# Kernel tuning notes

Measured on AMD Instinct MI355X. Metric: run time of the kernel, lower is better.

Reference implementation:

```python
import jax, jax.numpy as jnp
import numpy as np

ROPE_BASE = 10000.0


def _rope_tables(T, d, dtype):
    # inv_freq over even indices, emb = concat(freqs, freqs) -> [T, d]
    inv_freq = 1.0 / (ROPE_BASE ** (jnp.arange(0, d, 2, dtype=jnp.float32) / d))
    t = jnp.arange(T, dtype=jnp.float32)
    freqs = jnp.einsum('i,j->ij', t, inv_freq)          # [T, d/2]
    emb = jnp.concatenate([freqs, freqs], axis=-1)      # [T, d]
    return jnp.cos(emb).astype(dtype), jnp.sin(emb).astype(dtype)


def _rotate_half(x):
    d = x.shape[-1] // 2
    return jnp.concatenate([-x[..., d:], x[..., :d]], axis=-1)


def _apply_rope(x, cos, sin):
    # x: [B, T, H, Dh]; cos/sin: [T, Dh] broadcast over batch and heads
    c = cos[None, :, None, :]
    s = sin[None, :, None, :]
    return x * c + _rotate_half(x) * s


def setup_inputs() -> dict:
    key = jax.random.key(0)
    k1, k2, k3 = jax.random.split(key, 3)
    B, T, C = 2, 2048, 1024
    x = jax.random.normal(k1, (B, T, C), dtype=jnp.float32)
    # weights stored as [in, out] (transposed nn.Linear), scaled like torch init
    W_qkv = jax.random.normal(k2, (C, 3 * C), dtype=jnp.float32) * (C ** -0.5)
    W_proj = jax.random.normal(k3, (C, C), dtype=jnp.float32) * (C ** -0.5)
    return {'x': x, 'W_qkv': W_qkv, 'W_proj': W_proj}


def reference(x, W_qkv, W_proj):
    B, T, C = x.shape
    H = 16
    Dh = C // H
    qkv = x @ W_qkv                                   # [B, T, 3C]
    q, k, v = jnp.split(qkv, 3, axis=-1)
    q = q.reshape(B, T, H, Dh)
    k = k.reshape(B, T, H, Dh)
    v = v.reshape(B, T, H, Dh)
    cos, sin = _rope_tables(T, Dh, x.dtype)
    q = _apply_rope(q, cos, sin)
    k = _apply_rope(k, cos, sin)
    scale = 1.0 / jnp.sqrt(jnp.asarray(Dh, dtype=x.dtype))
    # causal SDPA: scores [B, H, T, T]
    scores = jnp.einsum('bqhd,bkhd->bhqk', q, k) * scale
    causal = jnp.tril(jnp.ones((T, T), dtype=bool))
    scores = jnp.where(causal[None, None], scores, jnp.asarray(-jnp.inf, dtype=scores.dtype))
    attn = jax.nn.softmax(scores, axis=-1)
    y = jnp.einsum('bhqk,bkhd->bqhd', attn, v).reshape(B, T, C)
    return y @ W_proj
```

## Files before the change

kernel.cpp:

```cpp
#include <hip/hip_runtime.h>
#include <cstdint>
#include <cstddef>

typedef __bf16 bf16;
typedef __bf16 bf16x2 __attribute__((ext_vector_type(2)));
typedef __bf16 bf16x4 __attribute__((ext_vector_type(4)));
typedef __bf16 bf16x8 __attribute__((ext_vector_type(8)));
typedef float  f32x4  __attribute__((ext_vector_type(4)));
typedef float  f32x16 __attribute__((ext_vector_type(16)));
typedef int    i32x4  __attribute__((ext_vector_type(4)));

__device__ __forceinline__ float fexp2(float x) {
  float r;
  asm("v_exp_f32 %0, %1" : "=v"(r) : "v"(x));
  return r;
}
__device__ __forceinline__ float m3(float a, float b, float c) {
  return fmaxf(fmaxf(a, b), c);
}

#define G2L(src, dst)                                                          \
  __builtin_amdgcn_global_load_lds(                                            \
      (const __attribute__((address_space(1))) unsigned int*)(src),            \
      (__attribute__((address_space(3))) unsigned int*)(dst), 16, 0, 0)

__global__ void k_conv_tables(const float* __restrict__ in, bf16* __restrict__ out,
                              float* __restrict__ cosT, float* __restrict__ sinT) {
  int bx = blockIdx.x;
  if (bx < 2048) {
    int i = (bx * 256 + threadIdx.x) * 8;
    float4 a = *(const float4*)(in + i);
    float4 b = *(const float4*)(in + i + 4);
    bf16x8 o;
    o[0] = (bf16)a.x; o[1] = (bf16)a.y; o[2] = (bf16)a.z; o[3] = (bf16)a.w;
    o[4] = (bf16)b.x; o[5] = (bf16)b.y; o[6] = (bf16)b.z; o[7] = (bf16)b.w;
    *(bf16x8*)(out + i) = o;
  } else {
    int i = (bx - 2048) * 256 + threadIdx.x;
    int t = i >> 5, j = i & 31;
    float inv = powf(10000.0f, -(float)j * (1.0f / 32.0f));
    float f = (float)t * inv;
    cosT[i] = cosf(f);
    sinT[i] = sinf(f);
  }
}

__global__ void k_transpose_w(const float* __restrict__ wqkv, bf16* __restrict__ wqkvt,
                              const float* __restrict__ wproj, bf16* __restrict__ wprojt) {
  __shared__ float tile[32][33];
  int bx = blockIdx.x;
  const float* in;
  bf16* out;
  int C;
  if (bx < 96) { in = wqkv; out = wqkvt; C = 3072; }
  else         { in = wproj; out = wprojt; C = 1024; bx -= 96; }
  const int R = 1024;
  int c0 = bx * 32, r0 = blockIdx.y * 32;
  int tx = threadIdx.x & 31, ty = threadIdx.x >> 5;
#pragma unroll
  for (int i = 0; i < 32; i += 8)
    tile[ty + i][tx] = in[(size_t)(r0 + ty + i) * C + c0 + tx];
  __syncthreads();
#pragma unroll
  for (int i = 0; i < 32; i += 8)
    out[(size_t)(c0 + ty + i) * R + r0 + tx] = (bf16)tile[tx][ty + i];
}

__global__ __launch_bounds__(256) void k_rope_v(const bf16* __restrict__ qkv,
                                                const float* __restrict__ cosT,
                                                const float* __restrict__ sinT,
                                                bf16* __restrict__ qr,
                                                bf16* __restrict__ kr,
                                                bf16* __restrict__ vt) {
  __shared__ bf16 tile[64][66];
  int bh = blockIdx.y;
  int t0 = blockIdx.x * 64;
  int b = bh >> 4, h = bh & 15;
  int tt = threadIdx.x >> 2, g = threadIdx.x & 3;
  int c4 = g * 16;
  const bf16* row = qkv + (size_t)(b * 2048 + t0 + tt) * 3072 + h * 64;
  bf16x8 v0 = *(const bf16x8*)(row + 2048 + c4);
  bf16x8 v1 = *(const bf16x8*)(row + 2048 + c4 + 8);
#pragma unroll
  for (int j = 0; j < 8; j++) { tile[tt][c4 + j] = v0[j]; tile[tt][c4 + 8 + j] = v1[j]; }
  int tglob = t0 + tt;
  size_t ob = ((size_t)bh * 2048 + tglob) * 64;
  const float QS = 0.125f * 1.44269504f;
  bf16x8 qlo = *(const bf16x8*)(row + g * 8);
  bf16x8 qhi = *(const bf16x8*)(row + 32 + g * 8);
  bf16x8 klo = *(const bf16x8*)(row + 1024 + g * 8);
  bf16x8 khi = *(const bf16x8*)(row + 1024 + 32 + g * 8);
  bf16x8 qo0, qo1, ko0, ko1;
#pragma unroll
  for (int j = 0; j < 8; j++) {
    float c = cosT[tglob * 32 + g * 8 + j], s = sinT[tglob * 32 + g * 8 + j];
    float ql = (float)qlo[j], qh = (float)qhi[j];
    float kl = (float)klo[j], kh = (float)khi[j];
    qo0[j] = (bf16)((ql * c - qh * s) * QS);
    qo1[j] = (bf16)((qh * c + ql * s) * QS);
    ko0[j] = (bf16)(kl * c - kh * s);
    ko1[j] = (bf16)(kh * c + kl * s);
  }
  *(bf16x8*)&qr[ob + g * 8]      = qo0;
  *(bf16x8*)&qr[ob + 32 + g * 8] = qo1;
  *(bf16x8*)&kr[ob + g * 8]      = ko0;
  *(bf16x8*)&kr[ob + 32 + g * 8] = ko1;
  __syncthreads();
  int d = threadIdx.x >> 2, tc0 = (threadIdx.x & 3) * 16;
  bf16x8 o0, o1;
#pragma unroll
  for (int j = 0; j < 8; j++) { o0[j] = tile[tc0 + j][d]; o1[j] = tile[tc0 + 8 + j][d]; }
  bf16* dst = vt + ((size_t)bh * 64 + d) * 2048 + t0 + tc0;
  *(bf16x8*)dst = o0;
  *(bf16x8*)(dst + 8) = o1;
}

template <int OUTF32>
__global__ __launch_bounds__(256) void k_gemm_bt(const bf16* __restrict__ A,
                                                 const bf16* __restrict__ Bt,
                                                 float* __restrict__ Cf, bf16* __restrict__ Cb,
                                                 int M, int N, int K) {
  __shared__ __align__(16) bf16 sA[128 * 64];
  __shared__ __align__(16) bf16 sB[128 * 64];
  int nwg = gridDim.x * gridDim.y;
  int idl = blockIdx.y * gridDim.x + blockIdx.x;
  int cpx = nwg >> 3;
  int swz = (idl & 7) * cpx + (idl >> 3);
  int bx = swz % gridDim.x, by = swz / gridDim.x;
  int m0 = by * 128, n0 = bx * 128;
  int t = threadIdx.x, lane = t & 63, w = t >> 6;
  int wr = w >> 1, wc = w & 1;
  int lr = lane & 15, q2 = lane >> 4;
  int srow8 = lane >> 3, pc8 = lane & 7;
  f32x4 acc[4][4] = {};
  for (int k0 = 0; k0 < K; k0 += 64) {
#pragma unroll
    for (int is = 0; is < 4; is++) {
      int r = w * 32 + is * 8 + srow8;
      int lc = pc8 ^ (r & 7);
      G2L(A + (size_t)(m0 + r) * K + k0 + lc * 8, &sA[(w * 32 + is * 8) * 64]);
    }
#pragma unroll
    for (int is = 0; is < 4; is++) {
      int r = w * 32 + is * 8 + srow8;
      int lc = pc8 ^ (r & 7);
      G2L(Bt + (size_t)(n0 + r) * K + k0 + lc * 8, &sB[(w * 32 + is * 8) * 64]);
    }
    __syncthreads();
#pragma unroll
    for (int ch = 0; ch < 2; ch++) {
      bf16x8 af[4], bfr[4];
#pragma unroll
      for (int i = 0; i < 4; i++) {
        int r = wr * 64 + i * 16 + lr;
        af[i] = *(const bf16x8*)&sA[r * 64 + (((ch * 4 + q2) ^ (r & 7)) * 8)];
      }
#pragma unroll
      for (int i = 0; i < 4; i++) {
        int r = wc * 64 + i * 16 + lr;
        bfr[i] = *(const bf16x8*)&sB[r * 64 + (((ch * 4 + q2) ^ (r & 7)) * 8)];
      }
#pragma unroll
      for (int mi = 0; mi < 4; mi++)
#pragma unroll
        for (int ni = 0; ni < 4; ni++)
          acc[mi][ni] = __builtin_amdgcn_mfma_f32_16x16x32_bf16(af[mi], bfr[ni], acc[mi][ni], 0, 0, 0);
    }
    __syncthreads();
  }
  int row_base = m0 + wr * 64, col_base = n0 + wc * 64;
#pragma unroll
  for (int mi = 0; mi < 4; mi++)
#pragma unroll
    for (int ni = 0; ni < 4; ni++) {
      int col = col_base + ni * 16 + lr;
#pragma unroll
      for (int r = 0; r < 4; r++) {
        int row = row_base + mi * 16 + q2 * 4 + r;
        float v = acc[mi][ni][r];
        if (OUTF32) Cf[(size_t)row * N + col] = v;
        else        Cb[(size_t)row * N + col] = (bf16)v;
      }
    }
}

__global__ __launch_bounds__(128) void k_flash_part(const bf16* __restrict__ qr,
                                                    const bf16* __restrict__ kr,
                                                    const bf16* __restrict__ vt,
                                                    bf16* __restrict__ Opart,
                                                    float* __restrict__ ml) {
  const int T = 2048;
  int id = blockIdx.x;
  int slot = id >> 5;
  int bh = id & 31;
  int qt = 31, c = 0;
  {
    int s = slot;
#pragma unroll 1
    for (int q = 31; q >= 0; --q) {
      int n = q / 6 + 1;
      if (s < n) { qt = q; c = s; break; }
      s -= n;
    }
  }
  int kt0 = c * 6;
  int kt1 = qt + 1 < kt0 + 6 ? qt + 1 : kt0 + 6;

  __shared__ __align__(16) bf16 sK[64 * 64];
  __shared__ __align__(16) bf16 sV[64 * 64];
  int t = threadIdx.x, lane = t & 63, w = t >> 6;
  int q31 = lane & 31, hi = lane >> 5;
  int srow8 = lane >> 3, pc8 = lane & 7;

  const bf16* Kbh = kr + (size_t)bh * T * 64;
  const bf16* Vbh = vt + (size_t)bh * 64 * T;

  int qwb = qt * 64 + w * 32;
  int qg = qwb + q31;
  const bf16* qrow = qr + ((size_t)bh * T + qg) * 64 + hi * 8;
  bf16x8 qf[4];
#pragma unroll
  for (int ks = 0; ks < 4; ks++) qf[ks] = *(const bf16x8*)(qrow + ks * 16);
  f32x16 o0 = {}, o1 = {};
  float m = -1e30f, l = 0.f;

  auto stage = [&](int kt) {
#pragma unroll
    for (int is = 0; is < 4; is++) {
      int r = w * 32 + is * 8 + srow8;
      int lc = pc8 ^ (r & 7);
      G2L(Kbh + (size_t)(kt * 64 + r) * 64 + lc * 8, &sK[(w * 32 + is * 8) * 64]);
    }
#pragma unroll
    for (int is = 0; is < 4; is++) {
      int d = w * 32 + is * 8 + srow8;
      int lc = pc8 ^ (d & 7);
      G2L(Vbh + (size_t)d * T + kt * 64 + lc * 8, &sV[(w * 32 + is * 8) * 64]);
    }
  };

  stage(kt0);
  for (int kt = kt0; kt < kt1; kt++) {
    asm volatile("s_waitcnt vmcnt(0)" ::: "memory");
    __builtin_amdgcn_s_barrier();
    asm volatile("" ::: "memory");
    __builtin_amdgcn_sched_barrier(0);
    f32x16 s[2];
    __builtin_amdgcn_s_setprio(1);
#pragma unroll
    for (int kb = 0; kb < 2; kb++) {
      f32x16 a = {};
      int krow = kb * 32 + q31;
#pragma unroll
      for (int ks = 0; ks < 4; ks++) {
        int ch = (ks * 2 + hi) ^ (krow & 7);
        bf16x8 kf = *(const bf16x8*)&sK[krow * 64 + ch * 8];
        a = __builtin_amdgcn_mfma_f32_32x32x16_bf16(kf, qf[ks], a, 0, 0, 0);
      }
      s[kb] = a;
    }
    __builtin_amdgcn_s_setprio(0);
    if (kt == qt) {
      int thr = qg - kt * 64;
#pragma unroll
      for (int kb = 0; kb < 2; kb++)
#pragma unroll
        for (int r = 0; r < 16; r++) {
          int koff = kb * 32 + (r & 3) + 8 * (r >> 2) + 4 * hi;
          if (koff > thr) s[kb][r] = -1e30f;
        }
    }
    float tm[16];
#pragma unroll
    for (int i = 0; i < 16; i++) tm[i] = fmaxf(s[0][i], s[1][i]);
    float a0 = m3(tm[0], tm[1], tm[2]);
    float a1 = m3(tm[3], tm[4], tm[5]);
    float a2 = m3(tm[6], tm[7], tm[8]);
    float a3 = m3(tm[9], tm[10], tm[11]);
    float a4 = m3(tm[12], tm[13], tm[14]);
    float b0 = m3(a0, a1, tm[15]);
    float b1 = m3(a2, a3, a4);
    float px = fmaxf(b0, b1);
    px = fmaxf(px, __shfl_xor(px, 32, 64));
    float mn = fmaxf(m, px);
    float alpha = fexp2(m - mn);
    m = mn;
    float ts[16];
#pragma unroll
    for (int i = 0; i < 16; i++) {
      float p0 = fexp2(s[0][i] - m);
      float p1 = fexp2(s[1][i] - m);
      s[0][i] = p0;
      s[1][i] = p1;
      ts[i] = p0 + p1;
    }
#pragma unroll
    for (int st = 8; st > 0; st >>= 1)
#pragma unroll
      for (int i = 0; i < st; i++) ts[i] += ts[i + st];
    float rs = ts[0];
    rs += __shfl_xor(rs, 32, 64);
    l = l * alpha + rs;
    int pw[4][4];
#pragma unroll
    for (int kb = 0; kb < 2; kb++) {
      int wd[8];
#pragma unroll
      for (int g = 0; g < 4; g++) {
        bf16x2 a, cc;
        a[0] = (bf16)s[kb][4 * g + 0]; a[1] = (bf16)s[kb][4 * g + 1];
        cc[0] = (bf16)s[kb][4 * g + 2]; cc[1] = (bf16)s[kb][4 * g + 3];
        wd[2 * g]     = __builtin_bit_cast(int, a);
        wd[2 * g + 1] = __builtin_bit_cast(int, cc);
      }
      asm volatile("v_permlane32_swap_b32 %0, %1" : "+v"(wd[0]), "+v"(wd[2]));
      asm volatile("v_permlane32_swap_b32 %0, %1" : "+v"(wd[1]), "+v"(wd[3]));
      asm volatile("v_permlane32_swap_b32 %0, %1" : "+v"(wd[4]), "+v"(wd[6]));
      asm volatile("v_permlane32_swap_b32 %0, %1" : "+v"(wd[5]), "+v"(wd[7]));
      pw[2 * kb][0] = wd[0]; pw[2 * kb][1] = wd[1];
      pw[2 * kb][2] = wd[2]; pw[2 * kb][3] = wd[3];
      pw[2 * kb + 1][0] = wd[4]; pw[2 * kb + 1][1] = wd[5];
      pw[2 * kb + 1][2] = wd[6]; pw[2 * kb + 1][3] = wd[7];
    }
#pragma unroll
    for (int r = 0; r < 16; r++) { o0[r] *= alpha; o1[r] *= alpha; }
    __builtin_amdgcn_s_setprio(1);
#pragma unroll
    for (int ks = 0; ks < 4; ks++) {
      i32x4 pv = {pw[ks][0], pw[ks][1], pw[ks][2], pw[ks][3]};
      bf16x8 pb = __builtin_bit_cast(bf16x8, pv);
      {
        int drow = q31;
        int ch = (ks * 2 + hi) ^ (drow & 7);
        bf16x8 vf = *(const bf16x8*)&sV[drow * 64 + ch * 8];
        o0 = __builtin_amdgcn_mfma_f32_32x32x16_bf16(vf, pb, o0, 0, 0, 0);
      }
      {
        int drow = 32 + q31;
        int ch = (ks * 2 + hi) ^ (drow & 7);
        bf16x8 vf = *(const bf16x8*)&sV[drow * 64 + ch * 8];
        o1 = __builtin_amdgcn_mfma_f32_32x32x16_bf16(vf, pb, o1, 0, 0, 0);
      }
    }
    __builtin_amdgcn_s_setprio(0);
    asm volatile("" ::: "memory");
    __builtin_amdgcn_s_barrier();
    asm volatile("" ::: "memory");
    if (kt + 1 < kt1) stage(kt + 1);
  }
  int qloc = w * 32 + q31;
  bf16* Ob = Opart + (size_t)id * 4096 + qloc * 64;
#pragma unroll
  for (int g = 0; g < 4; g++) {
    bf16x4 v0, v1;
#pragma unroll
    for (int j = 0; j < 4; j++) {
      v0[j] = (bf16)o0[4 * g + j];
      v1[j] = (bf16)o1[4 * g + j];
    }
    *(bf16x4*)&Ob[8 * g + 4 * hi]      = v0;
    *(bf16x4*)&Ob[32 + 8 * g + 4 * hi] = v1;
  }
  if (hi == 0) {
    ml[(size_t)id * 128 + qloc]      = m;
    ml[(size_t)id * 128 + 64 + qloc] = l;
  }
}

__global__ __launch_bounds__(256) void k_combine(const bf16* __restrict__ Opart,
                                                 const float* __restrict__ ml,
                                                 bf16* __restrict__ attn) {
  int bhqt = blockIdx.x;
  int bh = bhqt & 31, qt = bhqt >> 5;
  int b = bh >> 4, h = bh & 15;
  int nch = qt / 6 + 1;
  int slot0 = 0;
#pragma unroll 1
  for (int q = 31; q > qt; --q) slot0 += q / 6 + 1;
  int t = threadIdx.x;
  int q = t >> 2, ds = (t & 3) * 16;
  float M = -1e30f;
  for (int c = 0; c < nch; c++)
    M = fmaxf(M, ml[(size_t)((slot0 + c) * 32 + bh) * 128 + q]);
  float acc[16] = {};
  float L = 0.f;
  for (int c = 0; c < nch; c++) {
    int p = (slot0 + c) * 32 + bh;
    float wgt = fexp2(ml[(size_t)p * 128 + q] - M);
    L += wgt * ml[(size_t)p * 128 + 64 + q];
    const bf16* row = Opart + (size_t)p * 4096 + q * 64 + ds;
    bf16x8 a0 = *(const bf16x8*)row;
    bf16x8 a1 = *(const bf16x8*)(row + 8);
#pragma unroll
    for (int i = 0; i < 8; i++) {
      acc[i]     += wgt * (float)a0[i];
      acc[i + 8] += wgt * (float)a1[i];
    }
  }
  float Linv = 1.0f / L;
  bf16x8 w0, w1;
#pragma unroll
  for (int i = 0; i < 8; i++) {
    w0[i] = (bf16)(acc[i] * Linv);
    w1[i] = (bf16)(acc[i + 8] * Linv);
  }
  bf16* dst = attn + ((size_t)(b * 2048) + qt * 64 + q) * 1024 + h * 64 + ds;
  *(bf16x8*)dst = w0;
  *(bf16x8*)(dst + 8) = w1;
}

extern "C" void kernel_launch(void* const* d_in, const int* in_sizes, int n_in,
                              void* d_out, int out_size, void* d_ws, size_t ws_size,
                              hipStream_t stream) {
  const float* x     = (const float*)d_in[0];
  const float* Wqkv  = (const float*)d_in[1];
  const float* Wproj = (const float*)d_in[2];
  float* outp = (float*)d_out;
  const int B = 2, T = 2048, C = 1024;
  const int M = B * T;

  char* ws = (char*)d_ws;
  size_t off = 0;
  auto alloc = [&](size_t bytes) {
    void* p = ws + off;
    off += (bytes + 255) & ~(size_t)255;
    return p;
  };
  bf16* xb     = (bf16*)alloc((size_t)M * C * 2);
  bf16* wprojt = (bf16*)alloc((size_t)C * C * 2);
  float* cosT  = (float*)alloc((size_t)T * 32 * 4);
  float* sinT  = (float*)alloc((size_t)T * 32 * 4);
  bf16* qkv    = (bf16*)alloc((size_t)M * 3 * C * 2);
  bf16* wqkvt  = (bf16*)alloc((size_t)3 * C * C * 2);
  bf16* qr     = (bf16*)alloc((size_t)M * C * 2);
  bf16* kr     = (bf16*)alloc((size_t)M * C * 2);
  bf16* vt     = (bf16*)alloc((size_t)M * C * 2);
  bf16* attn   = xb;
  bf16* Opart  = qkv;
  float* ml    = (float*)(qkv + (size_t)3264 * 4096);

  k_conv_tables<<<dim3(2304), dim3(256), 0, stream>>>(x, xb, cosT, sinT);
  k_transpose_w<<<dim3(128, 32), dim3(256), 0, stream>>>(Wqkv, wqkvt, Wproj, wprojt);
  k_gemm_bt<0><<<dim3(3 * C / 128, M / 128), dim3(256), 0, stream>>>(xb, wqkvt, (float*)nullptr, qkv, M, 3 * C, C);
  k_rope_v<<<dim3(T / 64, 32), dim3(256), 0, stream>>>(qkv, cosT, sinT, qr, kr, vt);
  k_flash_part<<<dim3(3264), dim3(128), 0, stream>>>(qr, kr, vt, Opart, ml);
  k_combine<<<dim3(1024), dim3(256), 0, stream>>>(Opart, ml, attn);
  k_gemm_bt<1><<<dim3(C / 128, M / 128), dim3(256), 0, stream>>>(attn, wprojt, outp, (bf16*)nullptr, M, C, C);
}
```

Before: 126.5 us.

## Fuse RoPE into QKV GEMM epilogue, merge prep kernels, skip combine for single-chunk tiles

Merges the input conversion, table generation and weight transpose into one prep launch. RoPE and the Q scaling are applied in the QKV GEMM epilogue, so the full QKV intermediate no longer takes a round trip through memory. A separate small kernel transposes V. Flash blocks that cover the whole key range for a query tile normalise and write the attention output directly, and the combine kernel only handles tiles from qt=6 onward. The cost is scattered 2-byte stores in the GEMM epilogue and more branching.

```diff
diff --git a/kernel.cpp b/kernel.cpp
--- a/kernel.cpp
+++ b/kernel.cpp
@@ -24,102 +24,56 @@
       (const __attribute__((address_space(1))) unsigned int*)(src),            \
       (__attribute__((address_space(3))) unsigned int*)(dst), 16, 0, 0)
 
-__global__ void k_conv_tables(const float* __restrict__ in, bf16* __restrict__ out,
-                              float* __restrict__ cosT, float* __restrict__ sinT) {
+__global__ void k_prep(const float* __restrict__ x, bf16* __restrict__ xb,
+                       float* __restrict__ cosT, float* __restrict__ sinT,
+                       const float* __restrict__ wqkv, bf16* __restrict__ wqkvt,
+                       const float* __restrict__ wproj, bf16* __restrict__ wprojt) {
+  __shared__ float tile[32][33];
   int bx = blockIdx.x;
   if (bx < 2048) {
     int i = (bx * 256 + threadIdx.x) * 8;
-    float4 a = *(const float4*)(in + i);
-    float4 b = *(const float4*)(in + i + 4);
+    float4 a = *(const float4*)(x + i);
+    float4 b = *(const float4*)(x + i + 4);
     bf16x8 o;
     o[0] = (bf16)a.x; o[1] = (bf16)a.y; o[2] = (bf16)a.z; o[3] = (bf16)a.w;
     o[4] = (bf16)b.x; o[5] = (bf16)b.y; o[6] = (bf16)b.z; o[7] = (bf16)b.w;
-    *(bf16x8*)(out + i) = o;
-  } else {
+    *(bf16x8*)(xb + i) = o;
+  } else if (bx < 2304) {
     int i = (bx - 2048) * 256 + threadIdx.x;
     int t = i >> 5, j = i & 31;
     float inv = powf(10000.0f, -(float)j * (1.0f / 32.0f));
     float f = (float)t * inv;
     cosT[i] = cosf(f);
     sinT[i] = sinf(f);
-  }
-}
-
-__global__ void k_transpose_w(const float* __restrict__ wqkv, bf16* __restrict__ wqkvt,
-                              const float* __restrict__ wproj, bf16* __restrict__ wprojt) {
-  __shared__ float tile[32][33];
-  int bx = blockIdx.x;
-  const float* in;
-  bf16* out;
-  int C;
-  if (bx < 96) { in = wqkv; out = wqkvt; C = 3072; }
-  else         { in = wproj; out = wprojt; C = 1024; bx -= 96; }
-  const int R = 1024;
-  int c0 = bx * 32, r0 = blockIdx.y * 32;
-  int tx = threadIdx.x & 31, ty = threadIdx.x >> 5;
-#pragma unroll
-  for (int i = 0; i < 32; i += 8)
-    tile[ty + i][tx] = in[(size_t)(r0 + ty + i) * C + c0 + tx];
-  __syncthreads();
-#pragma unroll
-  for (int i = 0; i < 32; i += 8)
-    out[(size_t)(c0 + ty + i) * R + r0 + tx] = (bf16)tile[tx][ty + i];
-}
-
-__global__ __launch_bounds__(256) void k_rope_v(const bf16* __restrict__ qkv,
-                                                const float* __restrict__ cosT,
-                                                const float* __restrict__ sinT,
-                                                bf16* __restrict__ qr,
-                                                bf16* __restrict__ kr,
-                                                bf16* __restrict__ vt) {
-  __shared__ bf16 tile[64][66];
-  int bh = blockIdx.y;
-  int t0 = blockIdx.x * 64;
-  int b = bh >> 4, h = bh & 15;
-  int tt = threadIdx.x >> 2, g = threadIdx.x & 3;
-  int c4 = g * 16;
-  const bf16* row = qkv + (size_t)(b * 2048 + t0 + tt) * 3072 + h * 64;
-  bf16x8 v0 = *(const bf16x8*)(row + 2048 + c4);
-  bf16x8 v1 = *(const bf16x8*)(row + 2048 + c4 + 8);
-#pragma unroll
-  for (int j = 0; j < 8; j++) { tile[tt][c4 + j] = v0[j]; tile[tt][c4 + 8 + j] = v1[j]; }
-  int tglob = t0 + tt;
-  size_t ob = ((size_t)bh * 2048 + tglob) * 64;
-  const float QS = 0.125f * 1.44269504f;
-  bf16x8 qlo = *(const bf16x8*)(row + g * 8);
-  bf16x8 qhi = *(const bf16x8*)(row + 32 + g * 8);
-  bf16x8 klo = *(const bf16x8*)(row + 1024 + g * 8);
-  bf16x8 khi = *(const bf16x8*)(row + 1024 + 32 + g * 8);
-  bf16x8 qo0, qo1, ko0, ko1;
-#pragma unroll
-  for (int j = 0; j < 8; j++) {
-    float c = cosT[tglob * 32 + g * 8 + j], s = sinT[tglob * 32 + g * 8 + j];
-    float ql = (float)qlo[j], qh = (float)qhi[j];
-    float kl = (float)klo[j], kh = (float)khi[j];
-    qo0[j] = (bf16)((ql * c - qh * s) * QS);
-    qo1[j] = (bf16)((qh * c + ql * s) * QS);
-    ko0[j] = (bf16)(kl * c - kh * s);
-    ko1[j] = (bf16)(kh * c + kl * s);
-  }
-  *(bf16x8*)&qr[ob + g * 8]      = qo0;
-  *(bf16x8*)&qr[ob + 32 + g * 8] = qo1;
-  *(bf16x8*)&kr[ob + g * 8]      = ko0;
-  *(bf16x8*)&kr[ob + 32 + g * 8] = ko1;
-  __syncthreads();
-  int d = threadIdx.x >> 2, tc0 = (threadIdx.x & 3) * 16;
-  bf16x8 o0, o1;
-#pragma unroll
-  for (int j = 0; j < 8; j++) { o0[j] = tile[tc0 + j][d]; o1[j] = tile[tc0 + 8 + j][d]; }
-  bf16* dst = vt + ((size_t)bh * 64 + d) * 2048 + t0 + tc0;
-  *(bf16x8*)dst = o0;
-  *(bf16x8*)(dst + 8) = o1;
-}
-
-template <int OUTF32>
-__global__ __launch_bounds__(256) void k_gemm_bt(const bf16* __restrict__ A,
-                                                 const bf16* __restrict__ Bt,
-                                                 float* __restrict__ Cf, bf16* __restrict__ Cb,
-                                                 int M, int N, int K) {
+  } else {
+    int tb = bx - 2304;
+    int ty = tb >> 7, tx = tb & 127;
+    const float* in;
+    bf16* out;
+    int C;
+    if (tx < 96) { in = wqkv; out = wqkvt; C = 3072; }
+    else         { in = wproj; out = wprojt; C = 1024; tx -= 96; }
+    const int R = 1024;
+    int c0 = tx * 32, r0 = ty * 32;
+    int lx = threadIdx.x & 31, ly = threadIdx.x >> 5;
+#pragma unroll
+    for (int i = 0; i < 32; i += 8)
+      tile[ly + i][lx] = in[(size_t)(r0 + ly + i) * C + c0 + lx];
+    __syncthreads();
+#pragma unroll
+    for (int i = 0; i < 32; i += 8)
+      out[(size_t)(c0 + ly + i) * R + r0 + lx] = (bf16)tile[lx][ly + i];
+  }
+}
+
+__global__ __launch_bounds__(256) void k_gemm_qkv(const bf16* __restrict__ A,
+                                                  const bf16* __restrict__ Bt,
+                                                  const float* __restrict__ cosT,
+                                                  const float* __restrict__ sinT,
+                                                  bf16* __restrict__ qr,
+                                                  bf16* __restrict__ kr,
+                                                  bf16* __restrict__ v_plain) {
+  const int K = 1024, N = 3072, T = 2048;
   __shared__ __align__(16) bf16 sA[128 * 64];
   __shared__ __align__(16) bf16 sB[128 * 64];
   int nwg = gridDim.x * gridDim.y;
@@ -169,6 +123,117 @@
     __syncthreads();
   }
   int row_base = m0 + wr * 64, col_base = n0 + wc * 64;
+  int sec = col_base >> 10;
+  int h = (col_base & 1023) >> 6;
+  if (sec < 2) {
+    bf16* dst = (sec == 0) ? qr : kr;
+    const float scl = (sec == 0) ? 0.125f * 1.44269504f : 1.0f;
+#pragma unroll
+    for (int mi = 0; mi < 4; mi++)
+#pragma unroll
+      for (int r = 0; r < 4; r++) {
+        int row = row_base + mi * 16 + q2 * 4 + r;
+        int b = row >> 11, tt = row & 2047;
+        size_t obase = ((size_t)(b * 16 + h) * T + tt) * 64;
+#pragma unroll
+        for (int ni = 0; ni < 2; ni++) {
+          int jl = ni * 16 + lr;
+          float c = cosT[tt * 32 + jl], s = sinT[tt * 32 + jl];
+          float vlo = acc[mi][ni][r], vhi = acc[mi][ni + 2][r];
+          dst[obase + jl]      = (bf16)((vlo * c - vhi * s) * scl);
+          dst[obase + jl + 32] = (bf16)((vhi * c + vlo * s) * scl);
+        }
+      }
+  } else {
+#pragma unroll
+    for (int mi = 0; mi < 4; mi++)
+#pragma unroll
+      for (int ni = 0; ni < 4; ni++) {
+        int col = h * 64 + ni * 16 + lr;
+#pragma unroll
+        for (int r = 0; r < 4; r++) {
+          int row = row_base + mi * 16 + q2 * 4 + r;
+          v_plain[(size_t)row * 1024 + col] = (bf16)acc[mi][ni][r];
+        }
+      }
+  }
+}
+
+__global__ __launch_bounds__(256) void k_vtrans(const bf16* __restrict__ v_plain,
+                                                bf16* __restrict__ vt) {
+  __shared__ bf16 tile[64][66];
+  int bh = blockIdx.y;
+  int t0 = blockIdx.x * 64;
+  int b = bh >> 4, h = bh & 15;
+  int tt = threadIdx.x >> 2, c4 = (threadIdx.x & 3) * 16;
+  const bf16* src = v_plain + (size_t)(b * 2048 + t0 + tt) * 1024 + h * 64 + c4;
+  bf16x8 v0 = *(const bf16x8*)src;
+  bf16x8 v1 = *(const bf16x8*)(src + 8);
+#pragma unroll
+  for (int j = 0; j < 8; j++) { tile[tt][c4 + j] = v0[j]; tile[tt][c4 + 8 + j] = v1[j]; }
+  __syncthreads();
+  int d = threadIdx.x >> 2, tc0 = (threadIdx.x & 3) * 16;
+  bf16x8 o0, o1;
+#pragma unroll
+  for (int j = 0; j < 8; j++) { o0[j] = tile[tc0 + j][d]; o1[j] = tile[tc0 + 8 + j][d]; }
+  bf16* dst = vt + ((size_t)bh * 64 + d) * 2048 + t0 + tc0;
+  *(bf16x8*)dst = o0;
+  *(bf16x8*)(dst + 8) = o1;
+}
+
+__global__ __launch_bounds__(256) void k_gemm_proj(const bf16* __restrict__ A,
+                                                   const bf16* __restrict__ Bt,
+                                                   float* __restrict__ Cf,
+                                                   int M, int N, int K) {
+  __shared__ __align__(16) bf16 sA[128 * 64];
+  __shared__ __align__(16) bf16 sB[128 * 64];
+  int nwg = gridDim.x * gridDim.y;
+  int idl = blockIdx.y * gridDim.x + blockIdx.x;
+  int cpx = nwg >> 3;
+  int swz = (idl & 7) * cpx + (idl >> 3);
+  int bx = swz % gridDim.x, by = swz / gridDim.x;
+  int m0 = by * 128, n0 = bx * 128;
+  int t = threadIdx.x, lane = t & 63, w = t >> 6;
+  int wr = w >> 1, wc = w & 1;
+  int lr = lane & 15, q2 = lane >> 4;
+  int srow8 = lane >> 3, pc8 = lane & 7;
+  f32x4 acc[4][4] = {};
+  for (int k0 = 0; k0 < K; k0 += 64) {
+#pragma unroll
+    for (int is = 0; is < 4; is++) {
+      int r = w * 32 + is * 8 + srow8;
+      int lc = pc8 ^ (r & 7);
+      G2L(A + (size_t)(m0 + r) * K + k0 + lc * 8, &sA[(w * 32 + is * 8) * 64]);
+    }
+#pragma unroll
+    for (int is = 0; is < 4; is++) {
+      int r = w * 32 + is * 8 + srow8;
+      int lc = pc8 ^ (r & 7);
+      G2L(Bt + (size_t)(n0 + r) * K + k0 + lc * 8, &sB[(w * 32 + is * 8) * 64]);
+    }
+    __syncthreads();
+#pragma unroll
+    for (int ch = 0; ch < 2; ch++) {
+      bf16x8 af[4], bfr[4];
+#pragma unroll
+      for (int i = 0; i < 4; i++) {
+        int r = wr * 64 + i * 16 + lr;
+        af[i] = *(const bf16x8*)&sA[r * 64 + (((ch * 4 + q2) ^ (r & 7)) * 8)];
+      }
+#pragma unroll
+      for (int i = 0; i < 4; i++) {
+        int r = wc * 64 + i * 16 + lr;
+        bfr[i] = *(const bf16x8*)&sB[r * 64 + (((ch * 4 + q2) ^ (r & 7)) * 8)];
+      }
+#pragma unroll
+      for (int mi = 0; mi < 4; mi++)
+#pragma unroll
+        for (int ni = 0; ni < 4; ni++)
+          acc[mi][ni] = __builtin_amdgcn_mfma_f32_16x16x32_bf16(af[mi], bfr[ni], acc[mi][ni], 0, 0, 0);
+    }
+    __syncthreads();
+  }
+  int row_base = m0 + wr * 64, col_base = n0 + wc * 64;
 #pragma unroll
   for (int mi = 0; mi < 4; mi++)
 #pragma unroll
@@ -177,9 +242,7 @@
 #pragma unroll
       for (int r = 0; r < 4; r++) {
         int row = row_base + mi * 16 + q2 * 4 + r;
-        float v = acc[mi][ni][r];
-        if (OUTF32) Cf[(size_t)row * N + col] = v;
-        else        Cb[(size_t)row * N + col] = (bf16)v;
+        Cf[(size_t)row * N + col] = acc[mi][ni][r];
       }
     }
 }
@@ -188,7 +251,8 @@
                                                     const bf16* __restrict__ kr,
                                                     const bf16* __restrict__ vt,
                                                     bf16* __restrict__ Opart,
-                                                    float* __restrict__ ml) {
+                                                    float* __restrict__ ml,
+                                                    bf16* __restrict__ attn) {
   const int T = 2048;
   int id = blockIdx.x;
   int slot = id >> 5;
@@ -348,22 +412,39 @@
     asm volatile("" ::: "memory");
     if (kt + 1 < kt1) stage(kt + 1);
   }
-  int qloc = w * 32 + q31;
-  bf16* Ob = Opart + (size_t)id * 4096 + qloc * 64;
-#pragma unroll
-  for (int g = 0; g < 4; g++) {
-    bf16x4 v0, v1;
-#pragma unroll
-    for (int j = 0; j < 4; j++) {
-      v0[j] = (bf16)o0[4 * g + j];
-      v1[j] = (bf16)o1[4 * g + j];
-    }
-    *(bf16x4*)&Ob[8 * g + 4 * hi]      = v0;
-    *(bf16x4*)&Ob[32 + 8 * g + 4 * hi] = v1;
-  }
-  if (hi == 0) {
-    ml[(size_t)id * 128 + qloc]      = m;
-    ml[(size_t)id * 128 + 64 + qloc] = l;
+  if (kt0 == 0 && kt1 == qt + 1) {
+    int b = bh >> 4, h = bh & 15;
+    float linv = 1.0f / l;
+    bf16* orow = attn + ((size_t)b * T + qg) * 1024 + h * 64;
+#pragma unroll
+    for (int g = 0; g < 4; g++) {
+      bf16x4 v0, v1;
+#pragma unroll
+      for (int j = 0; j < 4; j++) {
+        v0[j] = (bf16)(o0[4 * g + j] * linv);
+        v1[j] = (bf16)(o1[4 * g + j] * linv);
+      }
+      *(bf16x4*)&orow[8 * g + 4 * hi]      = v0;
+      *(bf16x4*)&orow[32 + 8 * g + 4 * hi] = v1;
+    }
+  } else {
+    int qloc = w * 32 + q31;
+    bf16* Ob = Opart + (size_t)id * 4096 + qloc * 64;
+#pragma unroll
+    for (int g = 0; g < 4; g++) {
+      bf16x4 v0, v1;
+#pragma unroll
+      for (int j = 0; j < 4; j++) {
+        v0[j] = (bf16)o0[4 * g + j];
+        v1[j] = (bf16)o1[4 * g + j];
+      }
+      *(bf16x4*)&Ob[8 * g + 4 * hi]      = v0;
+      *(bf16x4*)&Ob[32 + 8 * g + 4 * hi] = v1;
+    }
+    if (hi == 0) {
+      ml[(size_t)id * 128 + qloc]      = m;
+      ml[(size_t)id * 128 + 64 + qloc] = l;
+    }
   }
 }
 
@@ -371,7 +452,7 @@
                                                  const float* __restrict__ ml,
                                                  bf16* __restrict__ attn) {
   int bhqt = blockIdx.x;
-  int bh = bhqt & 31, qt = bhqt >> 5;
+  int bh = bhqt & 31, qt = 6 + (bhqt >> 5);
   int b = bh >> 4, h = bh & 15;
   int nch = qt / 6 + 1;
   int slot0 = 0;
@@ -430,20 +511,20 @@
   bf16* wprojt = (bf16*)alloc((size_t)C * C * 2);
   float* cosT  = (float*)alloc((size_t)T * 32 * 4);
   float* sinT  = (float*)alloc((size_t)T * 32 * 4);
-  bf16* qkv    = (bf16*)alloc((size_t)M * 3 * C * 2);
-  bf16* wqkvt  = (bf16*)alloc((size_t)3 * C * C * 2);
+  bf16* region = (bf16*)alloc((size_t)M * 3 * C * 2 + (size_t)3 * C * C * 2);
+  bf16* wqkvt  = region + (size_t)M * 3 * C;
   bf16* qr     = (bf16*)alloc((size_t)M * C * 2);
   bf16* kr     = (bf16*)alloc((size_t)M * C * 2);
   bf16* vt     = (bf16*)alloc((size_t)M * C * 2);
-  bf16* attn   = xb;
-  bf16* Opart  = qkv;
-  float* ml    = (float*)(qkv + (size_t)3264 * 4096);
-
-  k_conv_tables<<<dim3(2304), dim3(256), 0, stream>>>(x, xb, cosT, sinT);
-  k_transpose_w<<<dim3(128, 32), dim3(256), 0, stream>>>(Wqkv, wqkvt, Wproj, wprojt);
-  k_gemm_bt<0><<<dim3(3 * C / 128, M / 128), dim3(256), 0, stream>>>(xb, wqkvt, (float*)nullptr, qkv, M, 3 * C, C);
-  k_rope_v<<<dim3(T / 64, 32), dim3(256), 0, stream>>>(qkv, cosT, sinT, qr, kr, vt);
-  k_flash_part<<<dim3(3264), dim3(128), 0, stream>>>(qr, kr, vt, Opart, ml);
-  k_combine<<<dim3(1024), dim3(256), 0, stream>>>(Opart, ml, attn);
-  k_gemm_bt<1><<<dim3(C / 128, M / 128), dim3(256), 0, stream>>>(attn, wprojt, outp, (bf16*)nullptr, M, C, C);
-}
+  bf16* attn    = xb;
+  bf16* v_plain = region;
+  bf16* Opart   = region;
+  float* ml     = (float*)(region + (size_t)3264 * 4096);
+
+  k_prep<<<dim3(6400), dim3(256), 0, stream>>>(x, xb, cosT, sinT, Wqkv, wqkvt, Wproj, wprojt);
+  k_gemm_qkv<<<dim3(3 * C / 128, M / 128), dim3(256), 0, stream>>>(xb, wqkvt, cosT, sinT, qr, kr, v_plain);
+  k_vtrans<<<dim3(T / 64, 32), dim3(256), 0, stream>>>(v_plain, vt);
+  k_flash_part<<<dim3(3264), dim3(128), 0, stream>>>(qr, kr, vt, Opart, ml, attn);
+  k_combine<<<dim3(832), dim3(256), 0, stream>>>(Opart, ml, attn);
+  k_gemm_proj<<<dim3(C / 128, M / 128), dim3(256), 0, stream>>>(attn, wprojt, outp, M, C, C);
+}
```

New measurement: 130.0 us. 2.7% more time.
